# Performance work log

Hardware: AMD Instinct MI355X
Metric: run time of the kernel (lower is better)

The kernel has to match this reference:

```python
import jax, jax.numpy as jnp
import numpy as np

B, D, H = 8192, 256, 512


def setup_inputs() -> dict:
    key = jax.random.key(0)
    ks = jax.random.split(key, 25)
    inp = {
        "x": jax.random.normal(ks[0], (B, D), jnp.float32),
        "h_t": jax.random.normal(ks[1], (B, H), jnp.float32),
        "h_s": jax.random.normal(ks[2], (B, H), jnp.float32),
        "c_t": jax.random.normal(ks[3], (B, H), jnp.float32),
        "c_s": jax.random.normal(ks[4], (B, H), jnp.float32),
    }
    names = ["Ui", "Wti", "Wsi", "bi", "Us", "Wts", "Wss", "bs",
             "Ut", "Wtt", "Wst", "bt", "Uo", "Wto", "Wso", "bo",
             "Uc", "Wtc", "Wsc", "bc"]
    shapes = {"U": (D, H), "W": (H, H), "b": (H,)}
    scale = 0.02  # keep activations in a sane range
    for i, n in enumerate(names):
        s = shapes["U"] if n[0] == "U" else (shapes["b"] if n[0] == "b" else shapes["W"])
        inp[n] = jax.random.normal(ks[5 + i], s, jnp.float32) * scale
    return inp


def reference(x, h_t, h_s, c_t, c_s,
              Ui, Wti, Wsi, bi, Us, Wts, Wss, bs,
              Ut, Wtt, Wst, bt, Uo, Wto, Wso, bo,
              Uc, Wtc, Wsc, bc):
    # Fuse the 15 small GEMMs into 3 concatenated GEMMs: [B,D]@[D,5H] etc.
    U = jnp.concatenate([Ui, Us, Ut, Uo, Uc], axis=1)      # [D, 5H]
    Wt = jnp.concatenate([Wti, Wts, Wtt, Wto, Wtc], axis=1)  # [H, 5H]
    Ws = jnp.concatenate([Wsi, Wss, Wst, Wso, Wsc], axis=1)  # [H, 5H]
    b = jnp.concatenate([bi, bs, bt, bo, bc])                # [5H]
    gates = x @ U + h_t @ Wt + h_s @ Ws + b                  # [B, 5H]
    g_i, g_fs, g_ft, g_o, g_c = jnp.split(gates, 5, axis=1)
    i_n = jax.nn.sigmoid(g_i)
    f_s_n = jax.nn.sigmoid(g_fs)
    f_t_n = jax.nn.sigmoid(g_ft)
    o_n = jax.nn.sigmoid(g_o)
    c_n = jnp.tanh(g_c)
    c_h = i_n * c_n + f_t_n * c_t + f_s_n * c_s
    h = o_n * jnp.tanh(c_h)
    return (h, c_h)
```

## Files before the change

kernel.cpp:

```cpp
#include <hip/hip_runtime.h>
#include <hip/hip_bf16.h>
#include <cstdint>
#include <cstddef>

#define B_  8192
#define D_  256
#define H_  512
#define K_  1280
#define N_  2560
#define NT_ 320
#define BM_ 256
#define BK_ 64

typedef short short8  __attribute__((ext_vector_type(8)));
typedef float f32x4   __attribute__((ext_vector_type(4)));
typedef float f32x16  __attribute__((ext_vector_type(16)));

__device__ __forceinline__ float sigf(float x)     { return 1.f / (1.f + __expf(-x)); }
__device__ __forceinline__ float tanhfast(float x) { return 1.f - 2.f / (__expf(2.f * x) + 1.f); }

struct WPtrs {
    const float* U[5];
    const float* Wt[5];
    const float* Ws[5];
};

__global__ void prep_w_kernel(WPtrs p, __hip_bfloat16* __restrict__ WT) {
    __shared__ __hip_bfloat16 tile[64][66];
    int bid2 = blockIdx.x;
    int hblk = bid2 & 7;
    int kblk = (bid2 >> 3) % 20;
    int g    = bid2 / 160;
    int k0 = kblk * 64;
    int h0 = hblk * 64;
    const float* src; int kl0;
    if (k0 < 256)      { src = p.U[g];  kl0 = k0; }
    else if (k0 < 768) { src = p.Wt[g]; kl0 = k0 - 256; }
    else               { src = p.Ws[g]; kl0 = k0 - 768; }
    int tid = threadIdx.x;
    int tk = tid >> 6;
    int th = tid & 63;
    for (int r = 0; r < 16; ++r) {
        int kl = r * 4 + tk;
        tile[kl][th] = __float2bfloat16(src[(size_t)(kl0 + kl) * H_ + h0 + th]);
    }
    __syncthreads();
    for (int r = 0; r < 16; ++r) {
        int hl = r * 4 + tk;
        int h  = h0 + hl;
        int np = (h >> 5) * 160 + g * 32 + (h & 31);
        WT[(size_t)np * K_ + k0 + th] = tile[th][hl];
    }
}

#define GLD16(gp, lp)                                                              \
    __builtin_amdgcn_global_load_lds(                                              \
        (const __attribute__((address_space(1))) unsigned int*)(gp),               \
        (__attribute__((address_space(3))) unsigned int*)(lp), 16, 0, 0)

__global__ __launch_bounds__(512, 2) void gemm_fused_kernel(
    const float* __restrict__ x, const float* __restrict__ ht,
    const float* __restrict__ hs, const __hip_bfloat16* __restrict__ WT,
    const float* __restrict__ ct, const float* __restrict__ cs,
    const float* __restrict__ bi, const float* __restrict__ bfs,
    const float* __restrict__ bft, const float* __restrict__ bo,
    const float* __restrict__ bc, float* __restrict__ out) {
    __shared__ alignas(16) unsigned short sA[2][BM_ * BK_];
    __shared__ alignas(16) unsigned short sB[2][NT_ * BK_];

    int tid = threadIdx.x;
    int m0 = blockIdx.x * BM_;
    int n0 = blockIdx.y * NT_;
    int wid  = tid >> 6, lane = tid & 63;
    int wm   = wid >> 1;
    int wn   = wid & 1;
    int half = lane >> 5, l31 = lane & 31;
    int xr   = l31 & 7;

    int hg = blockIdx.y * 2 + wn;
    int h  = hg * 32 + l31;
    float Bi = bi[h], Bfs = bfs[h], Bft = bft[h], Bo = bo[h], Bc = bc[h];

    f32x16 acc[2][5];
#pragma unroll
    for (int i = 0; i < 2; ++i)
#pragma unroll
        for (int j = 0; j < 5; ++j)
            acc[i][j] = (f32x16)(0.f);

    int srow = tid >> 3;
    int pA   = tid & 7;
    int xk   = srow & 7;

    const __hip_bfloat16* bBase = WT + (size_t)(n0 + srow) * K_ + (pA ^ xk) * 8;
    int t8 = tid * 8;
#define STG_B(dst, koff)                                                          \
    do {                                                                          \
        _Pragma("unroll")                                                         \
        for (int r_ = 0; r_ < 5; ++r_)                                            \
            GLD16(bBase + (size_t)r_ * 64 * K_ + (koff), (dst) + r_ * 4096 + t8); \
    } while (0)

    int rowIdx = m0 + srow;
    const float* xB  = x  + (size_t)rowIdx * D_ + pA * 8;
    const float* htB = ht + (size_t)rowIdx * H_ + pA * 8;
    const float* hsB = hs + (size_t)rowIdx * H_ + pA * 8;
    int aWr = srow * 64 + (pA ^ xk) * 8;

#define A_SRC(k0n, aP, aStr)                                                      \
    do {                                                                          \
        if ((k0n) < 256)      { aP = xB + (k0n);        aStr = 64 * D_; }         \
        else if ((k0n) < 768) { aP = htB + ((k0n)-256); aStr = 64 * H_; }         \
        else                  { aP = hsB + ((k0n)-768); aStr = 64 * H_; }         \
    } while (0)

#define A_LOAD2(av, aP, aStr, r0_)                                                \
    do {                                                                          \
        av[0][0] = *(const f32x4*)((aP) + (size_t)((r0_)) * (aStr));              \
        av[0][1] = *(const f32x4*)((aP) + (size_t)((r0_)) * (aStr) + 4);          \
        av[1][0] = *(const f32x4*)((aP) + (size_t)((r0_) + 1) * (aStr));          \
        av[1][1] = *(const f32x4*)((aP) + (size_t)((r0_) + 1) * (aStr) + 4);      \
    } while (0)

#define A_CVTWR(dst, av, r0_)                                                     \
    do {                                                                          \
        _Pragma("unroll")                                                         \
        for (int q_ = 0; q_ < 2; ++q_) {                                          \
            union { short8 s; __hip_bfloat16 hh[8]; } o_;                         \
            o_.hh[0] = __float2bfloat16(av[q_][0][0]);                            \
            o_.hh[1] = __float2bfloat16(av[q_][0][1]);                            \
            o_.hh[2] = __float2bfloat16(av[q_][0][2]);                            \
            o_.hh[3] = __float2bfloat16(av[q_][0][3]);                            \
            o_.hh[4] = __float2bfloat16(av[q_][1][0]);                            \
            o_.hh[5] = __float2bfloat16(av[q_][1][1]);                            \
            o_.hh[6] = __float2bfloat16(av[q_][1][2]);                            \
            o_.hh[7] = __float2bfloat16(av[q_][1][3]);                            \
            *(short8*)((dst) + ((r0_) + q_) * 4096 + aWr) = o_.s;                 \
        }                                                                         \
    } while (0)

    int arow64[2], brow64[5];
#pragma unroll
    for (int i = 0; i < 2; ++i) arow64[i] = (wm * 64 + i * 32 + l31) * 64;
#pragma unroll
    for (int j = 0; j < 5; ++j) brow64[j] = (wn * 160 + j * 32 + l31) * 64;

#define KSTEP(ks_)                                                                     \
    do {                                                                               \
        int po_ = (((ks_) * 2 + half) ^ xr) * 8;                                       \
        short8 a0 = *(const short8*)(sAc + arow64[0] + po_);                           \
        short8 a1 = *(const short8*)(sAc + arow64[1] + po_);                           \
        short8 b0 = *(const short8*)(sBc + brow64[0] + po_);                           \
        short8 b1 = *(const short8*)(sBc + brow64[1] + po_);                           \
        short8 b2 = *(const short8*)(sBc + brow64[2] + po_);                           \
        short8 b3 = *(const short8*)(sBc + brow64[3] + po_);                           \
        short8 b4 = *(const short8*)(sBc + brow64[4] + po_);                           \
        __builtin_amdgcn_s_setprio(1);                                                 \
        acc[0][0] = __builtin_amdgcn_mfma_f32_32x32x16_bf16(a0, b0, acc[0][0], 0, 0, 0); \
        acc[1][0] = __builtin_amdgcn_mfma_f32_32x32x16_bf16(a1, b0, acc[1][0], 0, 0, 0); \
        acc[0][1] = __builtin_amdgcn_mfma_f32_32x32x16_bf16(a0, b1, acc[0][1], 0, 0, 0); \
        acc[1][1] = __builtin_amdgcn_mfma_f32_32x32x16_bf16(a1, b1, acc[1][1], 0, 0, 0); \
        acc[0][2] = __builtin_amdgcn_mfma_f32_32x32x16_bf16(a0, b2, acc[0][2], 0, 0, 0); \
        acc[1][2] = __builtin_amdgcn_mfma_f32_32x32x16_bf16(a1, b2, acc[1][2], 0, 0, 0); \
        acc[0][3] = __builtin_amdgcn_mfma_f32_32x32x16_bf16(a0, b3, acc[0][3], 0, 0, 0); \
        acc[1][3] = __builtin_amdgcn_mfma_f32_32x32x16_bf16(a1, b3, acc[1][3], 0, 0, 0); \
        acc[0][4] = __builtin_amdgcn_mfma_f32_32x32x16_bf16(a0, b4, acc[0][4], 0, 0, 0); \
        acc[1][4] = __builtin_amdgcn_mfma_f32_32x32x16_bf16(a1, b4, acc[1][4], 0, 0, 0); \
        __builtin_amdgcn_s_setprio(0);                                                 \
    } while (0)

    {
        STG_B(sB[0], 0);
        const float* aP; int aStr;
        A_SRC(0, aP, aStr);
        f32x4 av[2][2];
        A_LOAD2(av, aP, aStr, 0); A_CVTWR(sA[0], av, 0);
        A_LOAD2(av, aP, aStr, 2); A_CVTWR(sA[0], av, 2);
    }
    __syncthreads();

    const int nt = K_ / BK_;
    for (int t = 0; t < nt; ++t) {
        const int cur = t & 1;
        const unsigned short* sAc = sA[cur];
        const unsigned short* sBc = sB[cur];
        unsigned short* sAn = sA[cur ^ 1];
        unsigned short* sBn = sB[cur ^ 1];
        const bool pf = (t + 1 < nt);
        const int kon = (t + 1) * BK_;

        const float* aP = nullptr; int aStr = 0;
        f32x4 av[2][2];
        if (pf) {
            A_SRC(kon, aP, aStr);
            STG_B(sBn, kon);
            A_LOAD2(av, aP, aStr, 0);
        }
        KSTEP(0);
        KSTEP(1);
        if (pf) {
            A_CVTWR(sAn, av, 0);
            A_LOAD2(av, aP, aStr, 2);
        }
        KSTEP(2);
        KSTEP(3);
        if (pf) A_CVTWR(sAn, av, 2);
        __syncthreads();
    }
#undef KSTEP
#undef STG_B
#undef A_SRC
#undef A_LOAD2
#undef A_CVTWR

#pragma unroll
    for (int i = 0; i < 2; ++i) {
        int rbase = m0 + wm * 64 + i * 32 + 4 * half;
#pragma unroll
        for (int r = 0; r < 16; ++r) {
            int row = rbase + (r & 3) + 8 * (r >> 2);
            size_t idx = (size_t)row * H_ + h;
            float i_n  = sigf(acc[i][0][r] + Bi);
            float fs_n = sigf(acc[i][1][r] + Bfs);
            float ft_n = sigf(acc[i][2][r] + Bft);
            float o_n  = sigf(acc[i][3][r] + Bo);
            float c_n  = tanhfast(acc[i][4][r] + Bc);
            float ch   = i_n * c_n + ft_n * ct[idx] + fs_n * cs[idx];
            out[idx] = o_n * tanhfast(ch);
            out[(size_t)B_ * H_ + idx] = ch;
        }
    }
}

struct AllW {
    const float* U[5];
    const float* Wt[5];
    const float* Ws[5];
    const float* bias[5];
};

__global__ __launch_bounds__(512) void fallback_kernel(const float* __restrict__ x,
                                                       const float* __restrict__ ht,
                                                       const float* __restrict__ hs,
                                                       const float* __restrict__ ct,
                                                       const float* __restrict__ cs,
                                                       AllW w, float* __restrict__ out) {
    __shared__ float arow[K_];
    int b = blockIdx.x;
    int h = threadIdx.x;
    for (int k = h; k < K_; k += 512) {
        float v;
        if (k < D_)           v = x[b * D_ + k];
        else if (k < D_ + H_) v = ht[b * H_ + k - D_];
        else                  v = hs[b * H_ + k - D_ - H_];
        arow[k] = v;
    }
    __syncthreads();
    float g[5];
    for (int gi = 0; gi < 5; ++gi) {
        float s = w.bias[gi][h];
        const float* U = w.U[gi];
        for (int k = 0; k < D_; ++k) s += arow[k] * U[(size_t)k * H_ + h];
        const float* Wt = w.Wt[gi];
        for (int k = 0; k < H_; ++k) s += arow[D_ + k] * Wt[(size_t)k * H_ + h];
        const float* Ws = w.Ws[gi];
        for (int k = 0; k < H_; ++k) s += arow[D_ + H_ + k] * Ws[(size_t)k * H_ + h];
        g[gi] = s;
    }
    int idx = b * H_ + h;
    float i_n = sigf(g[0]), fs_n = sigf(g[1]), ft_n = sigf(g[2]), o_n = sigf(g[3]);
    float c_n = tanhfast(g[4]);
    float ch  = i_n * c_n + ft_n * ct[idx] + fs_n * cs[idx];
    out[idx] = o_n * tanhfast(ch);
    out[(size_t)B_ * H_ + idx] = ch;
}

extern "C" void kernel_launch(void* const* d_in, const int* in_sizes, int n_in,
                              void* d_out, int out_size, void* d_ws, size_t ws_size,
                              hipStream_t stream) {
    const float* x  = (const float*)d_in[0];
    const float* ht = (const float*)d_in[1];
    const float* hs = (const float*)d_in[2];
    const float* ct = (const float*)d_in[3];
    const float* cs = (const float*)d_in[4];

    WPtrs wp;
    AllW  aw;
    const float* bias[5];
    for (int g = 0; g < 5; ++g) {
        wp.U[g]  = (const float*)d_in[5 + g * 4 + 0];
        wp.Wt[g] = (const float*)d_in[5 + g * 4 + 1];
        wp.Ws[g] = (const float*)d_in[5 + g * 4 + 2];
        bias[g]  = (const float*)d_in[5 + g * 4 + 3];
        aw.U[g] = wp.U[g]; aw.Wt[g] = wp.Wt[g]; aw.Ws[g] = wp.Ws[g]; aw.bias[g] = bias[g];
    }
    float* out = (float*)d_out;

    size_t szW = (size_t)N_ * K_ * 2;

    if (ws_size >= szW) {
        __hip_bfloat16* WT = (__hip_bfloat16*)d_ws;

        prep_w_kernel<<<800, 256, 0, stream>>>(wp, WT);
        gemm_fused_kernel<<<dim3(B_ / BM_, N_ / NT_), 512, 0, stream>>>(
            x, ht, hs, WT, ct, cs, bias[0], bias[1], bias[2], bias[3], bias[4], out);
    } else {
        fallback_kernel<<<B_, 512, 0, stream>>>(x, ht, hs, ct, cs, aw, out);
    }
}
```

Baseline: 229.8 us.

## Fuse weight-prep into GEMM kernel with a grid-wide atomic barrier

Removes the separate weight-transpose/bf16-conversion kernel and has each of the 256 GEMM blocks convert a share of the weight tiles into the workspace first. A global atomic counter barrier then holds every block until all 256 have arrived, after which the GEMM runs as before with a 1D block index remapped to (m,n). This saves one kernel launch and the gap between the two kernels, but it adds a memset launch plus a spin barrier. The barrier relies on all 256 blocks being co-resident and has a timeout that could let a block read incomplete weights.

```diff
diff --git a/kernel.cpp b/kernel.cpp
--- a/kernel.cpp
+++ b/kernel.cpp
@@ -25,42 +25,15 @@
     const float* Ws[5];
 };
 
-__global__ void prep_w_kernel(WPtrs p, __hip_bfloat16* __restrict__ WT) {
-    __shared__ __hip_bfloat16 tile[64][66];
-    int bid2 = blockIdx.x;
-    int hblk = bid2 & 7;
-    int kblk = (bid2 >> 3) % 20;
-    int g    = bid2 / 160;
-    int k0 = kblk * 64;
-    int h0 = hblk * 64;
-    const float* src; int kl0;
-    if (k0 < 256)      { src = p.U[g];  kl0 = k0; }
-    else if (k0 < 768) { src = p.Wt[g]; kl0 = k0 - 256; }
-    else               { src = p.Ws[g]; kl0 = k0 - 768; }
-    int tid = threadIdx.x;
-    int tk = tid >> 6;
-    int th = tid & 63;
-    for (int r = 0; r < 16; ++r) {
-        int kl = r * 4 + tk;
-        tile[kl][th] = __float2bfloat16(src[(size_t)(kl0 + kl) * H_ + h0 + th]);
-    }
-    __syncthreads();
-    for (int r = 0; r < 16; ++r) {
-        int hl = r * 4 + tk;
-        int h  = h0 + hl;
-        int np = (h >> 5) * 160 + g * 32 + (h & 31);
-        WT[(size_t)np * K_ + k0 + th] = tile[th][hl];
-    }
-}
-
 #define GLD16(gp, lp)                                                              \
     __builtin_amdgcn_global_load_lds(                                              \
         (const __attribute__((address_space(1))) unsigned int*)(gp),               \
         (__attribute__((address_space(3))) unsigned int*)(lp), 16, 0, 0)
 
-__global__ __launch_bounds__(512, 2) void gemm_fused_kernel(
+__global__ __launch_bounds__(512, 2) void fused_kernel(
     const float* __restrict__ x, const float* __restrict__ ht,
-    const float* __restrict__ hs, const __hip_bfloat16* __restrict__ WT,
+    const float* __restrict__ hs, WPtrs wp, __hip_bfloat16* __restrict__ WT,
+    unsigned int* __restrict__ cnt,
     const float* __restrict__ ct, const float* __restrict__ cs,
     const float* __restrict__ bi, const float* __restrict__ bfs,
     const float* __restrict__ bft, const float* __restrict__ bo,
@@ -69,15 +42,67 @@
     __shared__ alignas(16) unsigned short sB[2][NT_ * BK_];
 
     int tid = threadIdx.x;
-    int m0 = blockIdx.x * BM_;
-    int n0 = blockIdx.y * NT_;
+    int bid = blockIdx.x;
+
+    {
+        __hip_bfloat16* tbase = reinterpret_cast<__hip_bfloat16*>(&sA[0][0]);
+        int half_sel = (tid >= 256) ? 1 : 0;
+        __hip_bfloat16* tile = tbase + half_sel * (64 * 66);
+        int tid8 = tid & 255;
+        int tk = tid8 >> 6, th = tid8 & 63;
+        int hb = bid * 2 + half_sel;
+        for (int uu = 0; uu < 2; ++uu) {
+            int u = hb + uu * 512;
+            bool act = (u < 800);
+            const float* src = nullptr; int kl0 = 0, k0u = 0, h0u = 0, gu = 0;
+            if (act) {
+                int hblk = u & 7;
+                int kblk = (u >> 3) % 20;
+                gu = u / 160;
+                k0u = kblk * 64; h0u = hblk * 64;
+                if (k0u < 256)      { src = wp.U[gu];  kl0 = k0u; }
+                else if (k0u < 768) { src = wp.Wt[gu]; kl0 = k0u - 256; }
+                else                { src = wp.Ws[gu]; kl0 = k0u - 768; }
+                for (int r = 0; r < 16; ++r) {
+                    int kl = r * 4 + tk;
+                    tile[kl * 66 + th] =
+                        __float2bfloat16(src[(size_t)(kl0 + kl) * H_ + h0u + th]);
+                }
+            }
+            __syncthreads();
+            if (act) {
+                for (int r = 0; r < 16; ++r) {
+                    int hl = r * 4 + tk;
+                    int hh = h0u + hl;
+                    int np = (hh >> 5) * 160 + gu * 32 + (hh & 31);
+                    WT[(size_t)np * K_ + k0u + th] = tile[th * 66 + hl];
+                }
+            }
+            __syncthreads();
+        }
+    }
+
+    if (tid == 0) {
+        __threadfence();
+        atomicAdd(cnt, 1u);
+        long long t0 = clock64();
+        while (__hip_atomic_load(cnt, __ATOMIC_RELAXED, __HIP_MEMORY_SCOPE_AGENT) < 256u) {
+            __builtin_amdgcn_s_sleep(32);
+            if (clock64() - t0 > 60000000LL) break;
+        }
+        __threadfence();
+    }
+    __syncthreads();
+
+    int m0 = (bid & 31) * BM_;
+    int n0 = (bid >> 5) * NT_;
     int wid  = tid >> 6, lane = tid & 63;
     int wm   = wid >> 1;
     int wn   = wid & 1;
     int half = lane >> 5, l31 = lane & 31;
     int xr   = l31 & 7;
 
-    int hg = blockIdx.y * 2 + wn;
+    int hg = (bid >> 5) * 2 + wn;
     int h  = hg * 32 + l31;
     float Bi = bi[h], Bfs = bfs[h], Bft = bft[h], Bo = bo[h], Bc = bc[h];
 
@@ -296,14 +321,16 @@
     }
     float* out = (float*)d_out;
 
-    size_t szW = (size_t)N_ * K_ * 2;
-
-    if (ws_size >= szW) {
-        __hip_bfloat16* WT = (__hip_bfloat16*)d_ws;
-
-        prep_w_kernel<<<800, 256, 0, stream>>>(wp, WT);
-        gemm_fused_kernel<<<dim3(B_ / BM_, N_ / NT_), 512, 0, stream>>>(
-            x, ht, hs, WT, ct, cs, bias[0], bias[1], bias[2], bias[3], bias[4], out);
+    size_t szW    = (size_t)N_ * K_ * 2;
+    size_t cntOff = (szW + 127) & ~(size_t)127;
+
+    if (ws_size >= cntOff + 128) {
+        __hip_bfloat16* WT  = (__hip_bfloat16*)d_ws;
+        unsigned int*   cnt = (unsigned int*)((char*)d_ws + cntOff);
+        hipMemsetAsync(cnt, 0, 128, stream);
+        fused_kernel<<<256, 512, 0, stream>>>(
+            x, ht, hs, wp, WT, cnt, ct, cs,
+            bias[0], bias[1], bias[2], bias[3], bias[4], out);
     } else {
         fallback_kernel<<<B_, 512, 0, stream>>>(x, ht, hs, ct, cs, aw, out);
     }
```

Measured after the change: 253.6 us. 10.4% more time.
